# Optimization experiments

Hardware: AMD Instinct MI355X
Metric: run time of the kernel (lower is better)

## Reference

```python
import jax, jax.numpy as jnp
import numpy as np

EPS = 1e-12  # torch F.normalize default eps

def _l2norm(x):
    n = jnp.sqrt(jnp.sum(x * x, axis=-1, keepdims=True))
    return x / jnp.maximum(n, EPS)

def setup_inputs() -> dict:
    key = jax.random.key(0)
    k1, k2, k3 = jax.random.split(key, 3)
    N, S, D = 65536, 2048, 512
    return {
        "query": jax.random.normal(k1, (N, D), dtype=jnp.float32),
        "keys": jax.random.normal(k2, (S, D), dtype=jnp.float32),
        "values": jax.random.normal(k3, (S, D), dtype=jnp.float32),
    }

def reference(query, keys, values):
    q = _l2norm(query)            # [N, D]
    k = _l2norm(keys)             # [S, D]
    scores = jnp.einsum('nd,sd->ns', q, k)   # [N, S] cosine scores
    attn = jax.nn.softmax(scores, axis=-1)   # [N, S]
    return jnp.einsum('ns,sd->nd', attn, values)  # [N, D]
```

## Files before the change

kernel.cpp:

```cpp
#include <hip/hip_runtime.h>
#include <hip/hip_bf16.h>

typedef __attribute__((ext_vector_type(8))) short short8;
typedef __attribute__((ext_vector_type(4))) float f32x4;
typedef __attribute__((ext_vector_type(2))) unsigned int u32x2;

constexpr int D_DIM = 512;
constexpr int S_DIM = 2048;

static __device__ __forceinline__ unsigned short f2bf(float f) {
  __hip_bfloat16 h = __float2bfloat16(f);
  return *reinterpret_cast<unsigned short*>(&h);
}

#define GLP(p) ((const __attribute__((address_space(1))) unsigned int*)(p))
#define LDP(p) ((__attribute__((address_space(3))) unsigned int*)(p))

static __device__ __forceinline__ void blockbar() {
  asm volatile("" ::: "memory");
  __builtin_amdgcn_s_barrier();
  asm volatile("" ::: "memory");
}

static __device__ __forceinline__ void xcd_remap(int gx, int gy, int& bx, int& by) {
  const int nwg = gx * gy;
  int lin = by * gx + bx;
  if ((nwg & 7) == 0) {
    const int cpx = nwg >> 3;
    lin = (lin & 7) * cpx + (lin >> 3);
  }
  bx = lin % gx;
  by = lin / gx;
}

__global__ void k_norm(const float* __restrict__ K, ushort* __restrict__ Kn) {
  const int row = blockIdx.x * 4 + (threadIdx.x >> 6);
  const int l   = threadIdx.x & 63;
  const float* src = K + (size_t)row * D_DIM + l * 8;
  float4 v0 = *(const float4*)(src);
  float4 v1 = *(const float4*)(src + 4);
  float ss = v0.x*v0.x + v0.y*v0.y + v0.z*v0.z + v0.w*v0.w
           + v1.x*v1.x + v1.y*v1.y + v1.z*v1.z + v1.w*v1.w;
  #pragma unroll
  for (int off = 1; off < 64; off <<= 1) ss += __shfl_xor(ss, off, 64);
  const float sc = 1.0f / fmaxf(sqrtf(ss), 1e-12f);
  float f[8] = {v0.x,v0.y,v0.z,v0.w,v1.x,v1.y,v1.z,v1.w};
  unsigned uu[4];
  #pragma unroll
  for (int i = 0; i < 4; ++i)
    uu[i] = (unsigned)f2bf(f[2*i]*sc) | ((unsigned)f2bf(f[2*i+1]*sc) << 16);
  *(uint4*)(Kn + (size_t)row * D_DIM + l*8) = make_uint4(uu[0],uu[1],uu[2],uu[3]);
}

__global__ void k_transpose_v(const float* __restrict__ V, ushort* __restrict__ Vt) {
  __shared__ float tile[64][65];
  const int s0 = blockIdx.x * 64;
  const int d0 = blockIdx.y * 64;
  const int tj = threadIdx.x & 63;
  const int ti = threadIdx.x >> 6;
  #pragma unroll
  for (int k = 0; k < 16; ++k) {
    int s = ti + 4*k;
    tile[s][tj] = V[(size_t)(s0+s) * D_DIM + d0 + tj];
  }
  __syncthreads();
  #pragma unroll
  for (int k = 0; k < 16; ++k) {
    int d = ti + 4*k;
    Vt[(size_t)(d0+d) * S_DIM + s0 + tj] = f2bf(tile[tj][d]);
  }
}

__global__ __launch_bounds__(512, 2) void gemm1_bt(
    const ushort* __restrict__ A, const ushort* __restrict__ B,
    int aStride, int bStride,
    int NT,
    ushort* __restrict__ Pout, float* __restrict__ rowsum,
    int ldC)
{
  __shared__ ushort lds[2][4][8192];
  char* ldsb = (char*)&lds[0][0][0];

  const int tid = threadIdx.x;
  const int w   = tid >> 6;
  const int l   = tid & 63;
  const int lhi = l >> 4;
  const int llo = l & 15;
  const int wm  = w >> 2;
  const int wn  = w & 3;
  int bx = blockIdx.x, by = blockIdx.y;
  xcd_remap(gridDim.x, gridDim.y, bx, by);
  const size_t m0 = (size_t)bx * 256;
  const size_t n0 = (size_t)by * 256;

  const char* Ab = (const char*)A;
  const char* Bb = (const char*)B;

  const int srow = tid >> 3;
  const int scb  = (tid & 7) * 16;
  auto stage = [&](int buf, int slot, int t) {
    const char* src; int stride; size_t r0;
    if (slot < 2) { src = Ab; stride = aStride; r0 = m0 + (size_t)slot * 128; }
    else          { src = Bb; stride = bStride; r0 = n0 + (size_t)(slot - 2) * 128; }
    char* lbase = ldsb + ((buf*4 + slot) * 16384) + w * 1024;
    {
      const int row = srow;
      const char* g = src + (r0 + row) * (size_t)stride + t*128 + (scb ^ ((row & 7) << 4));
      __builtin_amdgcn_global_load_lds(GLP(g), LDP(lbase), 16, 0, 0);
    }
    {
      const int row = srow + 64;
      const char* g = src + (r0 + row) * (size_t)stride + t*128 + (scb ^ ((row & 7) << 4));
      __builtin_amdgcn_global_load_lds(GLP(g), LDP(lbase + 8192), 16, 0, 0);
    }
  };

  const unsigned swz = (unsigned)((l & 7) << 4);
  short8 ar[4][2], br01[2][2], br23[2][2];
  f32x4 acc[8][4] = {};

  const char* aBase0 = ldsb + wm * 16384;
  const char* bBase0 = ldsb + (2 + (wn >> 1)) * 16384;
  const unsigned bRow0 = (unsigned)((wn & 1) * 64);

  auto readA = [&](int buf, int rfB) {
    const char* base = aBase0 + buf * 65536;
    #pragma unroll
    for (int rf = 0; rf < 4; ++rf)
      #pragma unroll
      for (int kk = 0; kk < 2; ++kk) {
        unsigned off = (unsigned)(((rfB + rf) * 16 + llo) * 128)
                     + (((unsigned)(kk*64 + lhi*16)) ^ swz);
        ar[rf][kk] = *(const short8*)(base + off);
      }
  };
  auto readB = [&](int buf, int cfB, short8 (&br)[2][2]) {
    const char* base = bBase0 + buf * 65536;
    #pragma unroll
    for (int c = 0; c < 2; ++c)
      #pragma unroll
      for (int kk = 0; kk < 2; ++kk) {
        unsigned off = (unsigned)((bRow0 + (cfB + c) * 16 + llo) * 128)
                     + (((unsigned)(kk*64 + lhi*16)) ^ swz);
        br[c][kk] = *(const short8*)(base + off);
      }
  };
  auto quad = [&](int rfB, int cfB, short8 (&br)[2][2]) {
    __builtin_amdgcn_s_setprio(1);
    #pragma unroll
    for (int kk = 0; kk < 2; ++kk)
      #pragma unroll
      for (int rf = 0; rf < 4; ++rf)
        #pragma unroll
        for (int c = 0; c < 2; ++c)
          acc[rfB+rf][cfB+c] = __builtin_amdgcn_mfma_f32_16x16x32_bf16(
              ar[rf][kk], br[c][kk], acc[rfB+rf][cfB+c], 0, 0, 0);
    __builtin_amdgcn_s_setprio(0);
  };

  stage(0, 2, 0); stage(0, 0, 0); stage(0, 1, 0); stage(0, 3, 0);
  stage(1, 2, 1); stage(1, 0, 1);

  for (int t = 0; t < NT; ++t) {
    const int cur = t & 1, nxt = cur ^ 1;
    if (t + 1 < NT) asm volatile("s_waitcnt vmcnt(4)" ::: "memory");
    else            asm volatile("s_waitcnt vmcnt(0)" ::: "memory");
    blockbar();
    readA(cur, 0);
    readB(cur, 0, br01);
    if (t + 1 < NT) stage(nxt, 1, t + 1);
    quad(0, 0, br01);
    blockbar();
    readB(cur, 2, br23);
    if (t + 1 < NT) stage(nxt, 3, t + 1);
    quad(0, 2, br23);
    blockbar();
    readA(cur, 4);
    if (t + 2 < NT) stage(cur, 2, t + 2);
    quad(4, 2, br23);
    blockbar();
    if (t + 2 < NT) stage(cur, 0, t + 2);
    quad(4, 0, br01);
  }

  #pragma unroll
  for (int rf = 0; rf < 8; ++rf) {
    float e[4][4];
    #pragma unroll
    for (int cf = 0; cf < 4; ++cf)
      #pragma unroll
      for (int j = 0; j < 4; ++j)
        e[cf][j] = __expf(acc[rf][cf][j]);
    #pragma unroll
    for (int j = 0; j < 4; ++j) {
      const size_t m = m0 + wm*128 + rf*16 + lhi*4 + j;
      #pragma unroll
      for (int cf = 0; cf < 4; ++cf) {
        const size_t n = n0 + wn*64 + cf*16 + llo;
        Pout[m * (size_t)ldC + n] = f2bf(e[cf][j]);
      }
      float rp = (e[0][j] + e[1][j]) + (e[2][j] + e[3][j]);
      rp += __shfl_xor(rp, 1, 64);
      rp += __shfl_xor(rp, 2, 64);
      rp += __shfl_xor(rp, 4, 64);
      rp += __shfl_xor(rp, 8, 64);
      if (llo == 0) atomicAdd(&rowsum[m], rp);
    }
  }
}

__global__ __launch_bounds__(512, 2) void gemm2_bt(
    const ushort* __restrict__ A, const ushort* __restrict__ B,
    int aStride, int bStride,
    int NT,
    float* __restrict__ Oout, const float* __restrict__ rowsum,
    int ldC)
{
  __shared__ ushort lds[3][3][8192];
  char* ldsb = (char*)&lds[0][0][0];

  const int tid = threadIdx.x;
  const int w   = tid >> 6;
  const int l   = tid & 63;
  const int lhi = l >> 4;
  const int llo = l & 15;
  const int wm  = w >> 2;
  const int wn  = w & 3;
  int bx = blockIdx.x, by = blockIdx.y;
  xcd_remap(gridDim.x, gridDim.y, bx, by);
  const size_t m0 = (size_t)bx * 128;
  const size_t n0 = (size_t)by * 256;

  const char* Ab = (const char*)A;
  const char* Bb = (const char*)B;

  const int srow = tid >> 3;
  const int scb  = (tid & 7) * 16;
  auto stage = [&](int buf, int slot, int t) {
    const char* src; int stride; size_t r0;
    if (slot == 0) { src = Ab; stride = aStride; r0 = m0; }
    else           { src = Bb; stride = bStride; r0 = n0 + (size_t)(slot - 1) * 128; }
    char* lbase = ldsb + ((buf*3 + slot) * 16384) + w * 1024;
    {
      const int row = srow;
      const char* g = src + (r0 + row) * (size_t)stride + t*128 + (scb ^ ((row & 7) << 4));
      __builtin_amdgcn_global_load_lds(GLP(g), LDP(lbase), 16, 0, 0);
    }
    {
      const int row = srow + 64;
      const char* g = src + (r0 + row) * (size_t)stride + t*128 + (scb ^ ((row & 7) << 4));
      __builtin_amdgcn_global_load_lds(GLP(g), LDP(lbase + 8192), 16, 0, 0);
    }
  };

  const unsigned swz = (unsigned)((l & 7) << 4);
  short8 ar[4][2], br01[2][2], br23[2][2];
  f32x4 acc[4][4] = {};

  const unsigned aRow0 = (unsigned)(wm * 64);
  const int bSlot = 1 + (wn >> 1);
  const unsigned bRow0 = (unsigned)((wn & 1) * 64);

  auto readA = [&](int buf) {
    const char* base = ldsb + (buf*3) * 16384;
    #pragma unroll
    for (int rf = 0; rf < 4; ++rf)
      #pragma unroll
      for (int kk = 0; kk < 2; ++kk) {
        unsigned off = (unsigned)((aRow0 + rf*16 + llo) * 128)
                     + (((unsigned)(kk*64 + lhi*16)) ^ swz);
        ar[rf][kk] = *(const short8*)(base + off);
      }
  };
  auto readB = [&](int buf, int cfB, short8 (&br)[2][2]) {
    const char* base = ldsb + (buf*3 + bSlot) * 16384;
    #pragma unroll
    for (int c = 0; c < 2; ++c)
      #pragma unroll
      for (int kk = 0; kk < 2; ++kk) {
        unsigned off = (unsigned)((bRow0 + (cfB + c) * 16 + llo) * 128)
                     + (((unsigned)(kk*64 + lhi*16)) ^ swz);
        br[c][kk] = *(const short8*)(base + off);
      }
  };
  auto quad = [&](int cfB, short8 (&br)[2][2]) {
    __builtin_amdgcn_s_setprio(1);
    #pragma unroll
    for (int kk = 0; kk < 2; ++kk)
      #pragma unroll
      for (int rf = 0; rf < 4; ++rf)
        #pragma unroll
        for (int c = 0; c < 2; ++c)
          acc[rf][cfB+c] = __builtin_amdgcn_mfma_f32_16x16x32_bf16(
              ar[rf][kk], br[c][kk], acc[rf][cfB+c], 0, 0, 0);
    __builtin_amdgcn_s_setprio(0);
  };

  stage(0, 0, 0); stage(0, 1, 0); stage(0, 2, 0);
  stage(1, 0, 1); stage(1, 1, 1); stage(1, 2, 1);

  for (int t = 0; t < NT; ++t) {
    const int cur = t % 3, nx2 = (t + 2) % 3;
    if (t + 1 < NT) asm volatile("s_waitcnt vmcnt(6)" ::: "memory");
    else            asm volatile("s_waitcnt vmcnt(0)" ::: "memory");
    blockbar();
    readA(cur);
    readB(cur, 0, br01);
    if (t + 2 < NT) { stage(nx2, 0, t + 2); stage(nx2, 1, t + 2); }
    quad(0, br01);
    blockbar();
    readB(cur, 2, br23);
    if (t + 2 < NT) stage(nx2, 2, t + 2);
    quad(2, br23);
  }

  #pragma unroll
  for (int rf = 0; rf < 4; ++rf)
    #pragma unroll
    for (int j = 0; j < 4; ++j) {
      const size_t m = m0 + wm*64 + rf*16 + lhi*4 + j;
      const float inv = 1.0f / rowsum[m];
      #pragma unroll
      for (int cf = 0; cf < 4; ++cf) {
        const size_t n = n0 + wn*64 + cf*16 + llo;
        Oout[m * (size_t)ldC + n] = acc[rf][cf][j] * inv;
      }
    }
}

constexpr int BMf = 64, BHf = 256, NHf = S_DIM / BHf, NWf = 8;
constexpr int PBUFf = BMf * BHf * 2;

__global__ __launch_bounds__(512, 2) void attn_fused(
    const float* __restrict__ Q, const ushort* __restrict__ Kn,
    const ushort* __restrict__ Vt, float* __restrict__ out)
{
  __shared__ ushort q_s[BMf * D_DIM];
  __shared__ ushort p_s[2 * BMf * BHf];
  __shared__ float  rs_lds[NWf * BMf];
  __shared__ float  rs_tot[BMf];
  char* qb = (char*)q_s;
  char* pb = (char*)p_s;
  const int tid = threadIdx.x;
  const int w   = tid >> 6;
  const int l   = tid & 63;
  const int lhi = l >> 4;
  const int llo = l & 15;
  const size_t q0 = (size_t)blockIdx.x * BMf;
  {
    const int row = tid >> 3;
    const int c   = tid & 7;
    const unsigned swzr = (unsigned)((row & 7) << 4);
    const float4* src = (const float4*)(Q + (q0 + row) * D_DIM);
    float4 t[16];
    float ss = 0.f;
    #pragma unroll
    for (int i = 0; i < 16; ++i) {
      t[i] = src[c + i*8];
      ss += t[i].x*t[i].x + t[i].y*t[i].y + t[i].z*t[i].z + t[i].w*t[i].w;
    }
    ss += __shfl_xor(ss, 1, 64);
    ss += __shfl_xor(ss, 2, 64);
    ss += __shfl_xor(ss, 4, 64);
    const float sc = 1.0f / fmaxf(sqrtf(ss), 1e-12f);
    #pragma unroll
    for (int i = 0; i < 16; ++i) {
      u32x2 pv;
      pv[0] = (unsigned)f2bf(t[i].x*sc) | ((unsigned)f2bf(t[i].y*sc) << 16);
      pv[1] = (unsigned)f2bf(t[i].z*sc) | ((unsigned)f2bf(t[i].w*sc) << 16);
      unsigned byte = (unsigned)(row*1024) + (((unsigned)(c*8 + i*64)) ^ swzr);
      *(u32x2*)(qb + byte) = pv;
    }
  }
  __syncthreads();
  f32x4 o[4][4] = {};
  float rs_acc[4] = {0.f, 0.f, 0.f, 0.f};
  const unsigned swz = (unsigned)((l & 7) << 4);
  unsigned rowbQ[4], rowbP[4];
  #pragma unroll
  for (int qf = 0; qf < 4; ++qf) {
    rowbQ[qf] = (unsigned)((qf*16 + llo) * 1024);
    rowbP[qf] = (unsigned)((qf*16 + llo) * 512);
  }
  auto do_qkt = [&](int h, f32x4 (&sacc)[2][4]) {
    const short8* kp[2];
    #pragma unroll
    for (int kf = 0; kf < 2; ++kf)
      kp[kf] = (const short8*)(Kn + (size_t)(h*BHf + w*32 + kf*16 + llo) * D_DIM + lhi*8);
    __builtin_amdgcn_s_setprio(1);
    #pragma unroll
    for (int ks = 0; ks < 16; ++ks) {
      const unsigned off = ((unsigned)(ks*64 + lhi*16)) ^ swz;
      short8 a[2], b[4];
      #pragma unroll
      for (int kf = 0; kf < 2; ++kf) a[kf] = kp[kf][ks*4];
      #pragma unroll
      for (int qf = 0; qf < 4; ++qf)
        b[qf] = *(const short8*)(qb + (rowbQ[qf] + off));
      #pragma unroll
      for (int kf = 0; kf < 2; ++kf)
        #pragma unroll
        for (int qf = 0; qf < 4; ++qf)
          sacc[kf][qf] = __builtin_amdgcn_mfma_f32_16x16x32_bf16(a[kf], b[qf], sacc[kf][qf], 0, 0, 0);
    }
    __builtin_amdgcn_s_setprio(0);
  };
  auto do_exp = [&](f32x4 (&sacc)[2][4], u32x2 (&pk)[2][4]) {
    #pragma unroll
    for (int kf = 0; kf < 2; ++kf)
      #pragma unroll
      for (int qf = 0; qf < 4; ++qf) {
        float p0 = __expf(sacc[kf][qf][0]);
        float p1 = __expf(sacc[kf][qf][1]);
        float p2 = __expf(sacc[kf][qf][2]);
        float p3 = __expf(sacc[kf][qf][3]);
        rs_acc[qf] += (p0 + p1) + (p2 + p3);
        pk[kf][qf][0] = (unsigned)f2bf(p0) | ((unsigned)f2bf(p1) << 16);
        pk[kf][qf][1] = (unsigned)f2bf(p2) | ((unsigned)f2bf(p3) << 16);
      }
  };
  auto do_pwrite = [&](u32x2 (&pk)[2][4], char* buf) {
    #pragma unroll
    for (int kf = 0; kf < 2; ++kf)
      #pragma unroll
      for (int qf = 0; qf < 4; ++qf) {
        unsigned lin = (unsigned)(w*64 + kf*32 + lhi*8);
        *(u32x2*)(buf + rowbP[qf] + (lin ^ swz)) = pk[kf][qf];
      }
  };
  auto do_pv = [&](int h, const char* buf) {
    const short8* vp[4];
    #pragma unroll
    for (int df = 0; df < 4; ++df)
      vp[df] = (const short8*)(Vt + (size_t)(w*64 + df*16 + llo) * S_DIM + h*BHf + lhi*8);
    __builtin_amdgcn_s_setprio(1);
    #pragma unroll
    for (int ks = 0; ks < 8; ++ks) {
      const unsigned off = ((unsigned)(ks*64 + lhi*16)) ^ swz;
      short8 a[4], b[4];
      #pragma unroll
      for (int qf = 0; qf < 4; ++qf)
        a[qf] = *(const short8*)(buf + (rowbP[qf] + off));
      #pragma unroll
      for (int df = 0; df < 4; ++df) b[df] = vp[df][ks*4];
      #pragma unroll
      for (int qf = 0; qf < 4; ++qf)
        #pragma unroll
        for (int df = 0; df < 4; ++df)
          o[qf][df] = __builtin_amdgcn_mfma_f32_16x16x32_bf16(a[qf], b[df], o[qf][df], 0, 0, 0);
    }
    __builtin_amdgcn_s_setprio(0);
  };
  {
    f32x4 sacc[2][4] = {};
    do_qkt(0, sacc);
    u32x2 pk[2][4];
    do_exp(sacc, pk);
    do_pwrite(pk, pb + 0);
  }
  __syncthreads();
  for (int i = 0; i < NHf - 1; ++i) {
    f32x4 sacc[2][4] = {};
    do_qkt(i + 1, sacc);
    u32x2 pk[2][4];
    do_exp(sacc, pk);
    do_pv(i, pb + (i & 1) * PBUFf);
    do_pwrite(pk, pb + ((i + 1) & 1) * PBUFf);
    __syncthreads();
  }
  do_pv(NHf - 1, pb + ((NHf - 1) & 1) * PBUFf);
  #pragma unroll
  for (int qf = 0; qf < 4; ++qf) {
    float v = rs_acc[qf];
    v += __shfl_xor(v, 16, 64);
    v += __shfl_xor(v, 32, 64);
    if (l < 16) rs_lds[w*BMf + qf*16 + llo] = v;
  }
  __syncthreads();
  if (tid < BMf) {
    float tot = 0.f;
    #pragma unroll
    for (int ww = 0; ww < NWf; ++ww) tot += rs_lds[ww*BMf + tid];
    rs_tot[tid] = tot;
  }
  __syncthreads();
  #pragma unroll
  for (int qf = 0; qf < 4; ++qf)
    #pragma unroll
    for (int r = 0; r < 4; ++r) {
      const int query = qf*16 + lhi*4 + r;
      const float inv = 1.0f / rs_tot[query];
      #pragma unroll
      for (int df = 0; df < 4; ++df) {
        const int dim = w*64 + df*16 + llo;
        out[(q0 + query) * D_DIM + dim] = o[qf][df][r] * inv;
      }
    }
}

extern "C" void kernel_launch(void* const* d_in, const int* in_sizes, int n_in,
                              void* d_out, int out_size, void* d_ws, size_t ws_size,
                              hipStream_t stream) {
  const float* Q = (const float*)d_in[0];
  const float* K = (const float*)d_in[1];
  const float* V = (const float*)d_in[2];
  float* out = (float*)d_out;
  const int N = in_sizes[0] / D_DIM;

  ushort* Kn = (ushort*)d_ws;
  ushort* Vt = Kn + (size_t)S_DIM * D_DIM;
  char*   rest = (char*)(Vt + (size_t)D_DIM * S_DIM);
  const size_t base_bytes = (size_t)S_DIM * D_DIM * 2 * 2;
  const size_t avail = ws_size > base_bytes ? ws_size - base_bytes : 0;

  const size_t perRow = (size_t)D_DIM*2 + (size_t)S_DIM*2 + 4;
  int chunk = 0;
  const int cand[4] = {32768, 16384, 8192, 4096};
  for (int i = 0; i < 4; ++i)
    if ((size_t)cand[i] * perRow <= avail && (N % cand[i]) == 0) { chunk = cand[i]; break; }

  k_norm<<<S_DIM/4, 256, 0, stream>>>(K, Kn);
  k_transpose_v<<<dim3(S_DIM/64, D_DIM/64), 256, 0, stream>>>(V, Vt);

  if (chunk == 0) {
    attn_fused<<<N/BMf, 512, 0, stream>>>(Q, Kn, Vt, out);
    return;
  }

  ushort* Qn = (ushort*)rest;
  ushort* P  = Qn + (size_t)chunk * D_DIM;
  float* rowsum = (float*)(P + (size_t)chunk * S_DIM);

  for (int c = 0; c < N; c += chunk) {
    k_norm<<<chunk/4, 256, 0, stream>>>(Q + (size_t)c * D_DIM, Qn);
    hipMemsetAsync(rowsum, 0, (size_t)chunk * 4, stream);
    gemm1_bt<<<dim3(chunk/256, S_DIM/256), 512, 0, stream>>>(
        Qn, Kn, D_DIM*2, D_DIM*2, D_DIM/64, P, rowsum, S_DIM);
    gemm2_bt<<<dim3(chunk/128, D_DIM/256), 512, 0, stream>>>(
        P, Vt, S_DIM*2, S_DIM*2, S_DIM/64,
        out + (size_t)c * D_DIM, rowsum, D_DIM);
  }
}
```

Before: 395.2 us.

## Stage gemm1 epilogue through LDS for coalesced stores and drop XCD remap

The gemm1 epilogue now writes exp'd bf16 scores into a swizzled LDS tile, then copies the 256x256 tile to global memory with 16-byte coalesced stores instead of scattered 2-byte stores. Row-sum partials from the four column warps are combined in shared memory, so only one atomicAdd per row per block is issued instead of four. The XCD block remapping is removed from both GEMMs, which changes L2 locality across chiplets. The epilogue adds a barrier, and LDS reuse must not overlap with any outstanding async loads.

New measurement: 401.1 us. Within noise of the previous version (+1.5%).

```diff
diff --git a/kernel.cpp b/kernel.cpp
--- a/kernel.cpp
+++ b/kernel.cpp
@@ -20,17 +20,6 @@
   asm volatile("" ::: "memory");
   __builtin_amdgcn_s_barrier();
   asm volatile("" ::: "memory");
-}
-
-static __device__ __forceinline__ void xcd_remap(int gx, int gy, int& bx, int& by) {
-  const int nwg = gx * gy;
-  int lin = by * gx + bx;
-  if ((nwg & 7) == 0) {
-    const int cpx = nwg >> 3;
-    lin = (lin & 7) * cpx + (lin >> 3);
-  }
-  bx = lin % gx;
-  by = lin / gx;
 }
 
 __global__ void k_norm(const float* __restrict__ K, ushort* __restrict__ Kn) {
@@ -79,6 +68,7 @@
     int ldC)
 {
   __shared__ ushort lds[2][4][8192];
+  __shared__ float rs_part[4][256];
   char* ldsb = (char*)&lds[0][0][0];
 
   const int tid = threadIdx.x;
@@ -88,10 +78,8 @@
   const int llo = l & 15;
   const int wm  = w >> 2;
   const int wn  = w & 3;
-  int bx = blockIdx.x, by = blockIdx.y;
-  xcd_remap(gridDim.x, gridDim.y, bx, by);
-  const size_t m0 = (size_t)bx * 256;
-  const size_t n0 = (size_t)by * 256;
+  const size_t m0 = (size_t)blockIdx.x * 256;
+  const size_t n0 = (size_t)blockIdx.y * 256;
 
   const char* Ab = (const char*)A;
   const char* Bb = (const char*)B;
@@ -183,6 +171,7 @@
     quad(4, 0, br01);
   }
 
+  char* epib = ldsb;
   #pragma unroll
   for (int rf = 0; rf < 8; ++rf) {
     float e[4][4];
@@ -193,19 +182,37 @@
         e[cf][j] = __expf(acc[rf][cf][j]);
     #pragma unroll
     for (int j = 0; j < 4; ++j) {
-      const size_t m = m0 + wm*128 + rf*16 + lhi*4 + j;
+      const int mloc = wm*128 + rf*16 + lhi*4 + j;
+      const unsigned swzr = (unsigned)((mloc & 7) << 4);
       #pragma unroll
       for (int cf = 0; cf < 4; ++cf) {
-        const size_t n = n0 + wn*64 + cf*16 + llo;
-        Pout[m * (size_t)ldC + n] = f2bf(e[cf][j]);
+        const unsigned nb = (unsigned)((wn*64 + cf*16 + llo) * 2);
+        *(ushort*)(epib + mloc*512 + (nb ^ swzr)) = f2bf(e[cf][j]);
       }
       float rp = (e[0][j] + e[1][j]) + (e[2][j] + e[3][j]);
       rp += __shfl_xor(rp, 1, 64);
       rp += __shfl_xor(rp, 2, 64);
       rp += __shfl_xor(rp, 4, 64);
       rp += __shfl_xor(rp, 8, 64);
-      if (llo == 0) atomicAdd(&rowsum[m], rp);
-    }
+      if (llo == 0) rs_part[wn][mloc] = rp;
+    }
+  }
+  __syncthreads();
+
+  {
+    const int r0 = tid >> 5;
+    const unsigned ecb = (unsigned)((tid & 31) * 16);
+    #pragma unroll
+    for (int it = 0; it < 16; ++it) {
+      const int row = r0 + it*16;
+      const unsigned swzr = (unsigned)((row & 7) << 4);
+      uint4 v = *(const uint4*)(epib + row*512 + (ecb ^ swzr));
+      *(uint4*)((char*)Pout + ((m0 + row) * (size_t)ldC + n0) * 2 + ecb) = v;
+    }
+  }
+  if (tid < 256) {
+    float s = (rs_part[0][tid] + rs_part[1][tid]) + (rs_part[2][tid] + rs_part[3][tid]);
+    atomicAdd(&rowsum[m0 + tid], s);
   }
 }
 
@@ -226,10 +233,8 @@
   const int llo = l & 15;
   const int wm  = w >> 2;
   const int wn  = w & 3;
-  int bx = blockIdx.x, by = blockIdx.y;
-  xcd_remap(gridDim.x, gridDim.y, bx, by);
-  const size_t m0 = (size_t)bx * 128;
-  const size_t n0 = (size_t)by * 256;
+  const size_t m0 = (size_t)blockIdx.x * 128;
+  const size_t n0 = (size_t)blockIdx.y * 256;
 
   const char* Ab = (const char*)A;
   const char* Bb = (const char*)B;
```
